# Kernel tuning notes

Measured on AMD Instinct MI355X. Metric: run time of the kernel, lower is better.

The kernel has to match this reference:

```python
import jax, jax.numpy as jnp
import numpy as np

HEADS = 8
C_OUT = 256


def _gconv1x1(x, w, g):
    # x: (B, Cin, H, W); w: (Cout, Cin//g) -> grouped 1x1 conv, out (B, g, Cout//g, L)
    B, C, H, W = x.shape
    xr = x.reshape(B, g, C // g, H * W)
    wr = w.reshape(g, w.shape[0] // g, C // g)
    return jnp.einsum('god,bgdl->bgol', wr, xr)


def _sine_pe(d, L, dtype):
    # standard transformer sinusoidal PE laid out as (channels=d, positions=L)
    pos = jnp.arange(L, dtype=jnp.float32)
    i = jnp.arange(0, d, 2, dtype=jnp.float32)
    inv_freq = jnp.exp(-np.float32(np.log(10000.0)) * i / d)  # (d/2,)
    ang = inv_freq[:, None] * pos[None, :]                    # (d/2, L)
    pe = jnp.zeros((d, L), jnp.float32)
    pe = pe.at[0::2].set(jnp.sin(ang)).at[1::2].set(jnp.cos(ang))
    return pe.astype(dtype)


def setup_inputs() -> dict:
    key = jax.random.key(0)
    k1, k2, k3, k4 = jax.random.split(key, 4)
    B, Cin, H, W = 2, 256, 24, 24
    std = np.float32(np.sqrt(2.0 / C_OUT))  # kaiming_normal fan_out, relu gain
    x = jax.random.normal(k1, (B, Cin, H, W), jnp.float32)
    wq = jax.random.normal(k2, (C_OUT, Cin // HEADS), jnp.float32) * std
    wk = jax.random.normal(k3, (C_OUT, Cin // HEADS), jnp.float32) * std
    wv = jax.random.normal(k4, (C_OUT, Cin // HEADS), jnp.float32) * std
    return {"x": x, "wq": wq, "wk": wk, "wv": wv}


def reference(x, wq, wk, wv):
    B, Cin, H, W = x.shape
    g = HEADS
    d = C_OUT // g
    L = H * W
    q = _gconv1x1(x, wq, g)  # (B, g, d, L)
    k = _gconv1x1(x, wk, g)
    v = _gconv1x1(x, wv, g)
    # sinusoidal positional encoding added to keys over flattened spatial dim
    pe = _sine_pe(C_OUT, L, x.dtype)
    k = (k.reshape(B, C_OUT, L) + pe[None]).reshape(B, g, d, L)
    # NOTE: original torch code flattens batch AND heads into the attention dim
    qf = q.transpose(0, 1, 3, 2).reshape(-1, d)   # (N, d), N = B*g*L
    kf = k.transpose(2, 0, 1, 3).reshape(d, -1)   # (d, N)
    vf = v.transpose(0, 1, 3, 2).reshape(-1, d)   # (N, d)
    scale = np.float32(np.sqrt(g / C_OUT))        # = 1/sqrt(d)
    att = jax.nn.softmax(qf @ kf * scale, axis=-1)  # (N, N)
    out = att @ vf                                  # (N, d)
    out = out.reshape(B, g, L, d).transpose(0, 1, 3, 2).reshape(B, C_OUT, H, W)
    return out
```

## Files before the change

### kernel.cpp

```cpp
#include <hip/hip_runtime.h>
#include <hip/hip_bf16.h>


#define LSP   576
#define NROW  9216
#define DH    32
#define NW    16
#define KPW   (NROW / NW)
#define NTILE 9
#define PSTR  40
#define QB    36
#define SZ    ((size_t)NROW * DH)
#define SZP   (SZ + 4096)

typedef __attribute__((ext_vector_type(8))) short bh8;
typedef __attribute__((ext_vector_type(4))) float f4;

static __device__ __forceinline__ unsigned short f2bf(float x) {
    union { float f; unsigned int i; } w; w.f = x;
    unsigned int u = w.i;
    return (unsigned short)((u + 0x7fffu + ((u >> 16) & 1u)) >> 16);
}
static __device__ __forceinline__ unsigned int pkbf(float a, float b) {
    union { __hip_bfloat162 h2; unsigned int u; } w;
    w.h2 = __float22bfloat162_rn(make_float2(a, b));
    return w.u;
}
static __device__ __forceinline__ float fexp2(float x) {
#if __has_builtin(__builtin_amdgcn_exp2f)
    return __builtin_amdgcn_exp2f(x);
#else
    return exp2f(x);
#endif
}

#define MFMA(a, b, c) __builtin_amdgcn_mfma_f32_16x16x32_bf16(a, b, c, 0, 0, 0)

__global__ __launch_bounds__(256) void sa_proj_kernel(
    const float* __restrict__ x,
    const float* __restrict__ wq, const float* __restrict__ wk, const float* __restrict__ wv,
    unsigned short* __restrict__ Qhi, unsigned short* __restrict__ Khi,
    unsigned short* __restrict__ Vt)
{
    __shared__ __align__(16) float xs[32 * 40];
    __shared__ float vt[32 * 37];
    __shared__ float wqs[32 * 33], wks[32 * 33], wvs[32 * 33];
    const int t = threadIdx.x;
    const int bg = blockIdx.x >> 4;
    const int part = blockIdx.x & 15;
    const int g = bg & 7;
    const int l0 = part * 36;

    const float* xp = x + (size_t)bg * 32 * LSP + l0;
    for (int i = t; i < 32 * 9; i += 256) {
        int d = i / 9, seg = i % 9;
        *(float4*)(xs + d * 40 + seg * 4) = *(const float4*)(xp + d * LSP + seg * 4);
    }
    for (int i = t; i < 1024; i += 256) {
        int o = i >> 5, d = i & 31;
        wqs[o * 33 + d] = wq[(g * 32 + o) * 32 + d];
        wks[o * 33 + d] = wk[(g * 32 + o) * 32 + d];
        wvs[o * 33 + d] = wv[(g * 32 + o) * 32 + d];
    }
    __syncthreads();

    const float scale = 0.17677669529663687f * 1.4426950408889634f;
    for (int idx = t; idx < 32 * 36; idx += 256) {
        const int o = idx & 31;
        const int lloc = idx >> 5;
        const int l = l0 + lloc;
        float aq = 0.f, ak = 0.f, av = 0.f;
        #pragma unroll
        for (int d = 0; d < 32; d++) {
            const float xv = xs[d * 40 + lloc];
            aq = fmaf(wqs[o * 33 + d], xv, aq);
            ak = fmaf(wks[o * 33 + d], xv, ak);
            av = fmaf(wvs[o * 33 + d], xv, av);
        }
        aq *= scale;
        const int c = g * 32 + o;
        const float i2 = (float)(c & ~1);
        const float inv = __expf(-0.035977892078031968f * i2);
        float sv, cv;
        __sincosf(inv * (float)l, &sv, &cv);
        ak += (c & 1) ? cv : sv;

        const size_t row = (size_t)bg * LSP + l;
        Qhi[row * 32 + o] = f2bf(aq);
        Khi[row * 32 + o] = f2bf(ak);
        vt[o * 37 + lloc] = av;
    }
    __syncthreads();

    for (int idx = t; idx < 32 * 36; idx += 256) {
        const int d = idx / 36;
        const int cc = idx - d * 36;
        const int n = bg * LSP + l0 + cc;
        const int k = n & 31;
        const int cperm = (k < 16) ? ((k >> 2) * 8 + (k & 3))
                                   : (((k - 16) >> 2) * 8 + ((k - 16) & 3) + 4);
        Vt[(size_t)(n >> 5) * 1024 + d * 32 + cperm] = f2bf(vt[d * 37 + cc]);
    }
}

__global__ __launch_bounds__(1024, 4) void sa_attn_kernel(
    const unsigned short* __restrict__ Qhi, const unsigned short* __restrict__ Khi,
    const unsigned short* __restrict__ Vt, float* __restrict__ out)
{
    __shared__ __align__(16) unsigned short shm[NW * 48 * PSTR];
    const int t = threadIdx.x;
    const int wave = t >> 6, lane = t & 63;
    const int quad = lane >> 4, l16 = lane & 15;
    const int n0 = blockIdx.x * QB;

    unsigned short* psw = shm + wave * 48 * PSTR;

    const bh8 qh0 = *(const bh8*)(Qhi + (size_t)(n0 + l16) * DH + quad * 8);
    const bh8 qh1 = *(const bh8*)(Qhi + (size_t)(n0 + 16 + l16) * DH + quad * 8);
    const bh8 qh2 = *(const bh8*)(Qhi + (size_t)(n0 + 32 + l16) * DH + quad * 8);

    f4 o00 = {0.f,0.f,0.f,0.f}, o01 = {0.f,0.f,0.f,0.f};
    f4 o10 = {0.f,0.f,0.f,0.f}, o11 = {0.f,0.f,0.f,0.f};
    f4 o20 = {0.f,0.f,0.f,0.f}, o21 = {0.f,0.f,0.f,0.f};
    float ls0 = 0.f, ls1 = 0.f, ls2 = 0.f;
    const f4 zf = {0.f,0.f,0.f,0.f};

    const int kbase = wave * KPW;
    const int tile0 = kbase >> 5;

    bh8 kfa0 = *(const bh8*)(Khi + (size_t)(kbase + l16) * DH + quad * 8);
    bh8 kfa1 = *(const bh8*)(Khi + (size_t)(kbase + 16 + l16) * DH + quad * 8);
    bh8 kfb0 = *(const bh8*)(Khi + (size_t)(kbase + 32 + l16) * DH + quad * 8);
    bh8 kfb1 = *(const bh8*)(Khi + (size_t)(kbase + 48 + l16) * DH + quad * 8);
    bh8 vfa0 = *(const bh8*)(Vt + (size_t)tile0 * 1024 + l16 * 32 + quad * 8);
    bh8 vfa1 = *(const bh8*)(Vt + (size_t)tile0 * 1024 + (16 + l16) * 32 + quad * 8);
    bh8 vfb0 = *(const bh8*)(Vt + (size_t)(tile0 + 1) * 1024 + l16 * 32 + quad * 8);
    bh8 vfb1 = *(const bh8*)(Vt + (size_t)(tile0 + 1) * 1024 + (16 + l16) * 32 + quad * 8);

    for (int it = 0; it < NTILE; ++it) {
        const int tn = (it + 1 < NTILE) ? it + 1 : it;
        const int kna = kbase + tn * 64;

        f4 s00 = MFMA(kfa0, qh0, zf);
        f4 s01 = MFMA(kfa0, qh1, zf);
        f4 s02 = MFMA(kfa0, qh2, zf);
        f4 s10 = MFMA(kfa1, qh0, zf);
        f4 s11 = MFMA(kfa1, qh1, zf);
        f4 s12 = MFMA(kfa1, qh2, zf);
        kfa0 = *(const bh8*)(Khi + (size_t)(kna + l16) * DH + quad * 8);
        kfa1 = *(const bh8*)(Khi + (size_t)(kna + 16 + l16) * DH + quad * 8);

        uint4 w0, w1, w2;
        {
            float a = fexp2(s00[0]), b = fexp2(s00[1]),
                  c = fexp2(s00[2]), d = fexp2(s00[3]);
            ls0 += (a + b) + (c + d);
            w0.x = pkbf(a, b); w0.y = pkbf(c, d);
            a = fexp2(s10[0]); b = fexp2(s10[1]);
            c = fexp2(s10[2]); d = fexp2(s10[3]);
            ls0 += (a + b) + (c + d);
            w0.z = pkbf(a, b); w0.w = pkbf(c, d);
            a = fexp2(s01[0]); b = fexp2(s01[1]);
            c = fexp2(s01[2]); d = fexp2(s01[3]);
            ls1 += (a + b) + (c + d);
            w1.x = pkbf(a, b); w1.y = pkbf(c, d);
            a = fexp2(s11[0]); b = fexp2(s11[1]);
            c = fexp2(s11[2]); d = fexp2(s11[3]);
            ls1 += (a + b) + (c + d);
            w1.z = pkbf(a, b); w1.w = pkbf(c, d);
            a = fexp2(s02[0]); b = fexp2(s02[1]);
            c = fexp2(s02[2]); d = fexp2(s02[3]);
            ls2 += (a + b) + (c + d);
            w2.x = pkbf(a, b); w2.y = pkbf(c, d);
            a = fexp2(s12[0]); b = fexp2(s12[1]);
            c = fexp2(s12[2]); d = fexp2(s12[3]);
            ls2 += (a + b) + (c + d);
            w2.z = pkbf(a, b); w2.w = pkbf(c, d);
        }
        *(uint4*)(psw + l16 * PSTR + quad * 8) = w0;
        *(uint4*)(psw + (16 + l16) * PSTR + quad * 8) = w1;
        *(uint4*)(psw + (32 + l16) * PSTR + quad * 8) = w2;

        f4 b00 = MFMA(kfb0, qh0, zf);
        f4 b01 = MFMA(kfb0, qh1, zf);
        f4 b02 = MFMA(kfb0, qh2, zf);
        f4 b10 = MFMA(kfb1, qh0, zf);
        f4 b11 = MFMA(kfb1, qh1, zf);
        f4 b12 = MFMA(kfb1, qh2, zf);
        kfb0 = *(const bh8*)(Khi + (size_t)(kna + 32 + l16) * DH + quad * 8);
        kfb1 = *(const bh8*)(Khi + (size_t)(kna + 48 + l16) * DH + quad * 8);

        uint4 u0, u1, u2;
        {
            float a = fexp2(b00[0]), b = fexp2(b00[1]),
                  c = fexp2(b00[2]), d = fexp2(b00[3]);
            ls0 += (a + b) + (c + d);
            u0.x = pkbf(a, b); u0.y = pkbf(c, d);
            a = fexp2(b10[0]); b = fexp2(b10[1]);
            c = fexp2(b10[2]); d = fexp2(b10[3]);
            ls0 += (a + b) + (c + d);
            u0.z = pkbf(a, b); u0.w = pkbf(c, d);
            a = fexp2(b01[0]); b = fexp2(b01[1]);
            c = fexp2(b01[2]); d = fexp2(b01[3]);
            ls1 += (a + b) + (c + d);
            u1.x = pkbf(a, b); u1.y = pkbf(c, d);
            a = fexp2(b11[0]); b = fexp2(b11[1]);
            c = fexp2(b11[2]); d = fexp2(b11[3]);
            ls1 += (a + b) + (c + d);
            u1.z = pkbf(a, b); u1.w = pkbf(c, d);
            a = fexp2(b02[0]); b = fexp2(b02[1]);
            c = fexp2(b02[2]); d = fexp2(b02[3]);
            ls2 += (a + b) + (c + d);
            u2.x = pkbf(a, b); u2.y = pkbf(c, d);
            a = fexp2(b12[0]); b = fexp2(b12[1]);
            c = fexp2(b12[2]); d = fexp2(b12[3]);
            ls2 += (a + b) + (c + d);
            u2.z = pkbf(a, b); u2.w = pkbf(c, d);
        }

        {
            const bh8 pa0 = *(const bh8*)(psw + l16 * PSTR + quad * 8);
            const bh8 pa1 = *(const bh8*)(psw + (16 + l16) * PSTR + quad * 8);
            const bh8 pa2 = *(const bh8*)(psw + (32 + l16) * PSTR + quad * 8);
            o00 = MFMA(pa0, vfa0, o00); o01 = MFMA(pa0, vfa1, o01);
            o10 = MFMA(pa1, vfa0, o10); o11 = MFMA(pa1, vfa1, o11);
            o20 = MFMA(pa2, vfa0, o20); o21 = MFMA(pa2, vfa1, o21);
        }
        vfa0 = *(const bh8*)(Vt + (size_t)(tile0 + 2 * tn) * 1024 + l16 * 32 + quad * 8);
        vfa1 = *(const bh8*)(Vt + (size_t)(tile0 + 2 * tn) * 1024 + (16 + l16) * 32 + quad * 8);

        *(uint4*)(psw + l16 * PSTR + quad * 8) = u0;
        *(uint4*)(psw + (16 + l16) * PSTR + quad * 8) = u1;
        *(uint4*)(psw + (32 + l16) * PSTR + quad * 8) = u2;

        {
            const bh8 pb0 = *(const bh8*)(psw + l16 * PSTR + quad * 8);
            const bh8 pb1 = *(const bh8*)(psw + (16 + l16) * PSTR + quad * 8);
            const bh8 pb2 = *(const bh8*)(psw + (32 + l16) * PSTR + quad * 8);
            o00 = MFMA(pb0, vfb0, o00); o01 = MFMA(pb0, vfb1, o01);
            o10 = MFMA(pb1, vfb0, o10); o11 = MFMA(pb1, vfb1, o11);
            o20 = MFMA(pb2, vfb0, o20); o21 = MFMA(pb2, vfb1, o21);
        }
        vfb0 = *(const bh8*)(Vt + (size_t)(tile0 + 2 * tn + 1) * 1024 + l16 * 32 + quad * 8);
        vfb1 = *(const bh8*)(Vt + (size_t)(tile0 + 2 * tn + 1) * 1024 + (16 + l16) * 32 + quad * 8);
    }

    ls0 += __shfl_xor(ls0, 16); ls0 += __shfl_xor(ls0, 32);
    ls1 += __shfl_xor(ls1, 16); ls1 += __shfl_xor(ls1, 32);
    ls2 += __shfl_xor(ls2, 16); ls2 += __shfl_xor(ls2, 32);

    __syncthreads();
    float* mo = (float*)shm;
    float* mls = mo + 8 * 1536;
    const int mw = wave & 7;
    float* mp = mo + mw * 1536;
    if (wave < 8) {
        #pragma unroll
        for (int reg = 0; reg < 4; ++reg) {
            const int q0 = quad * 4 + reg;
            mp[l16 * 48 + q0]             = o00[reg];
            mp[(16 + l16) * 48 + q0]      = o01[reg];
            mp[l16 * 48 + 16 + q0]        = o10[reg];
            mp[(16 + l16) * 48 + 16 + q0] = o11[reg];
            mp[l16 * 48 + 32 + q0]        = o20[reg];
            mp[(16 + l16) * 48 + 32 + q0] = o21[reg];
        }
        if (quad == 0) {
            mls[mw * 48 + l16]      = ls0;
            mls[mw * 48 + 16 + l16] = ls1;
            mls[mw * 48 + 32 + l16] = ls2;
        }
    }
    __syncthreads();
    if (wave >= 8) {
        #pragma unroll
        for (int reg = 0; reg < 4; ++reg) {
            const int q0 = quad * 4 + reg;
            mp[l16 * 48 + q0]             += o00[reg];
            mp[(16 + l16) * 48 + q0]      += o01[reg];
            mp[l16 * 48 + 16 + q0]        += o10[reg];
            mp[(16 + l16) * 48 + 16 + q0] += o11[reg];
            mp[l16 * 48 + 32 + q0]        += o20[reg];
            mp[(16 + l16) * 48 + 32 + q0] += o21[reg];
        }
        if (quad == 0) {
            mls[mw * 48 + l16]      += ls0;
            mls[mw * 48 + 16 + l16] += ls1;
            mls[mw * 48 + 32 + l16] += ls2;
        }
    }
    __syncthreads();

    const int bg = n0 / LSP;
    const int l0 = n0 - bg * LSP;
    for (int c = t; c < 32 * QB; c += 1024) {
        const int d = c / QB;
        const int q = c - d * QB;
        float num = 0.f, den = 0.f;
        #pragma unroll
        for (int w2 = 0; w2 < 8; ++w2) {
            num += mo[w2 * 1536 + d * 48 + q];
            den += mls[w2 * 48 + q];
        }
        out[((size_t)(bg * 32 + d)) * LSP + l0 + q] = num / den;
    }
}

extern "C" void kernel_launch(void* const* d_in, const int* in_sizes, int n_in,
                              void* d_out, int out_size, void* d_ws, size_t ws_size,
                              hipStream_t stream) {
    (void)in_sizes; (void)n_in; (void)out_size; (void)ws_size;
    const float* x  = (const float*)d_in[0];
    const float* wq = (const float*)d_in[1];
    const float* wk = (const float*)d_in[2];
    const float* wv = (const float*)d_in[3];

    unsigned short* ws = (unsigned short*)d_ws;
    unsigned short* Qhi = ws;
    unsigned short* Khi = ws + SZP;
    unsigned short* Vt  = ws + 2 * SZP;
    float* out = (float*)d_out;

    sa_proj_kernel<<<256, 256, 0, stream>>>(x, wq, wk, wv, Qhi, Khi, Vt);
    sa_attn_kernel<<<256, 1024, 0, stream>>>(Qhi, Khi, Vt, out);
}
```

Baseline: 90.66 us.

## Fuse projection and attention into one cooperative kernel; compute row sums via MFMA

Merges the projection kernel into the attention kernel and separates the two phases with a cooperative-groups grid sync, launched via hipLaunchCooperativeKernel with 256 blocks of 1024 threads. This removes one kernel launch and the gap between launches. The softmax denominators are now accumulated by extra MFMAs against a ones vector instead of scalar adds and shuffles, moving VALU work onto the matrix units. The cost is a grid-wide barrier, a reliance on all 256 blocks being co-resident, and extra MFMA issue per tile.

```diff
diff --git a/kernel.cpp b/kernel.cpp
--- a/kernel.cpp
+++ b/kernel.cpp
@@ -1,5 +1,8 @@
 #include <hip/hip_runtime.h>
 #include <hip/hip_bf16.h>
+#include <hip/hip_cooperative_groups.h>
+
+namespace cg = cooperative_groups;
 
 
 #define LSP   576
@@ -36,79 +39,82 @@
 
 #define MFMA(a, b, c) __builtin_amdgcn_mfma_f32_16x16x32_bf16(a, b, c, 0, 0, 0)
 
-__global__ __launch_bounds__(256) void sa_proj_kernel(
+__global__ __launch_bounds__(1024, 4) void sa_fused_kernel(
     const float* __restrict__ x,
     const float* __restrict__ wq, const float* __restrict__ wk, const float* __restrict__ wv,
     unsigned short* __restrict__ Qhi, unsigned short* __restrict__ Khi,
-    unsigned short* __restrict__ Vt)
-{
-    __shared__ __align__(16) float xs[32 * 40];
-    __shared__ float vt[32 * 37];
-    __shared__ float wqs[32 * 33], wks[32 * 33], wvs[32 * 33];
-    const int t = threadIdx.x;
-    const int bg = blockIdx.x >> 4;
-    const int part = blockIdx.x & 15;
-    const int g = bg & 7;
-    const int l0 = part * 36;
-
-    const float* xp = x + (size_t)bg * 32 * LSP + l0;
-    for (int i = t; i < 32 * 9; i += 256) {
-        int d = i / 9, seg = i % 9;
-        *(float4*)(xs + d * 40 + seg * 4) = *(const float4*)(xp + d * LSP + seg * 4);
-    }
-    for (int i = t; i < 1024; i += 256) {
-        int o = i >> 5, d = i & 31;
-        wqs[o * 33 + d] = wq[(g * 32 + o) * 32 + d];
-        wks[o * 33 + d] = wk[(g * 32 + o) * 32 + d];
-        wvs[o * 33 + d] = wv[(g * 32 + o) * 32 + d];
-    }
-    __syncthreads();
-
-    const float scale = 0.17677669529663687f * 1.4426950408889634f;
-    for (int idx = t; idx < 32 * 36; idx += 256) {
-        const int o = idx & 31;
-        const int lloc = idx >> 5;
-        const int l = l0 + lloc;
-        float aq = 0.f, ak = 0.f, av = 0.f;
-        #pragma unroll
-        for (int d = 0; d < 32; d++) {
-            const float xv = xs[d * 40 + lloc];
-            aq = fmaf(wqs[o * 33 + d], xv, aq);
-            ak = fmaf(wks[o * 33 + d], xv, ak);
-            av = fmaf(wvs[o * 33 + d], xv, av);
-        }
-        aq *= scale;
-        const int c = g * 32 + o;
-        const float i2 = (float)(c & ~1);
-        const float inv = __expf(-0.035977892078031968f * i2);
-        float sv, cv;
-        __sincosf(inv * (float)l, &sv, &cv);
-        ak += (c & 1) ? cv : sv;
-
-        const size_t row = (size_t)bg * LSP + l;
-        Qhi[row * 32 + o] = f2bf(aq);
-        Khi[row * 32 + o] = f2bf(ak);
-        vt[o * 37 + lloc] = av;
-    }
-    __syncthreads();
-
-    for (int idx = t; idx < 32 * 36; idx += 256) {
-        const int d = idx / 36;
-        const int cc = idx - d * 36;
-        const int n = bg * LSP + l0 + cc;
-        const int k = n & 31;
-        const int cperm = (k < 16) ? ((k >> 2) * 8 + (k & 3))
-                                   : (((k - 16) >> 2) * 8 + ((k - 16) & 3) + 4);
-        Vt[(size_t)(n >> 5) * 1024 + d * 32 + cperm] = f2bf(vt[d * 37 + cc]);
-    }
-}
-
-__global__ __launch_bounds__(1024, 4) void sa_attn_kernel(
-    const unsigned short* __restrict__ Qhi, const unsigned short* __restrict__ Khi,
-    const unsigned short* __restrict__ Vt, float* __restrict__ out)
+    unsigned short* __restrict__ Vt, float* __restrict__ out)
 {
     __shared__ __align__(16) unsigned short shm[NW * 48 * PSTR];
     const int t = threadIdx.x;
+
+    {
+        float* xs  = (float*)shm;
+        float* vt  = xs + 32 * 40;
+        float* wqs = vt + 32 * 37;
+        float* wks = wqs + 32 * 33;
+        float* wvs = wks + 32 * 33;
+
+        const int bg = blockIdx.x >> 4;
+        const int part = blockIdx.x & 15;
+        const int g = bg & 7;
+        const int l0 = part * 36;
+
+        const float* xp = x + (size_t)bg * 32 * LSP + l0;
+        if (t < 288) {
+            const int d = t / 9, seg = t - d * 9;
+            *(float4*)(xs + d * 40 + seg * 4) = *(const float4*)(xp + d * LSP + seg * 4);
+        }
+        {
+            const int o = t >> 5, d = t & 31;
+            wqs[o * 33 + d] = wq[(g * 32 + o) * 32 + d];
+            wks[o * 33 + d] = wk[(g * 32 + o) * 32 + d];
+            wvs[o * 33 + d] = wv[(g * 32 + o) * 32 + d];
+        }
+        __syncthreads();
+
+        const float scale = 0.17677669529663687f * 1.4426950408889634f;
+        for (int idx = t; idx < 32 * 36; idx += 1024) {
+            const int o = idx & 31;
+            const int lloc = idx >> 5;
+            const int l = l0 + lloc;
+            float aq = 0.f, ak = 0.f, av = 0.f;
+            #pragma unroll
+            for (int d = 0; d < 32; d++) {
+                const float xv = xs[d * 40 + lloc];
+                aq = fmaf(wqs[o * 33 + d], xv, aq);
+                ak = fmaf(wks[o * 33 + d], xv, ak);
+                av = fmaf(wvs[o * 33 + d], xv, av);
+            }
+            aq *= scale;
+            const int c = g * 32 + o;
+            const float i2 = (float)(c & ~1);
+            const float inv = __expf(-0.035977892078031968f * i2);
+            float sv, cv;
+            __sincosf(inv * (float)l, &sv, &cv);
+            ak += (c & 1) ? cv : sv;
+
+            const size_t row = (size_t)bg * LSP + l;
+            Qhi[row * 32 + o] = f2bf(aq);
+            Khi[row * 32 + o] = f2bf(ak);
+            vt[o * 37 + lloc] = av;
+        }
+        __syncthreads();
+
+        for (int idx = t; idx < 32 * 36; idx += 1024) {
+            const int d = idx / 36;
+            const int cc = idx - d * 36;
+            const int n = bg * LSP + l0 + cc;
+            const int k = n & 31;
+            const int cperm = (k < 16) ? ((k >> 2) * 8 + (k & 3))
+                                       : (((k - 16) >> 2) * 8 + ((k - 16) & 3) + 4);
+            Vt[(size_t)(n >> 5) * 1024 + d * 32 + cperm] = f2bf(vt[d * 37 + cc]);
+        }
+    }
+
+    __threadfence();
+    cg::this_grid().sync();
+
     const int wave = t >> 6, lane = t & 63;
     const int quad = lane >> 4, l16 = lane & 15;
     const int n0 = blockIdx.x * QB;
@@ -119,10 +125,13 @@
     const bh8 qh1 = *(const bh8*)(Qhi + (size_t)(n0 + 16 + l16) * DH + quad * 8);
     const bh8 qh2 = *(const bh8*)(Qhi + (size_t)(n0 + 32 + l16) * DH + quad * 8);
 
+    const short oneb = (short)0x3F80;
+    const bh8 ones = {oneb, oneb, oneb, oneb, oneb, oneb, oneb, oneb};
+
     f4 o00 = {0.f,0.f,0.f,0.f}, o01 = {0.f,0.f,0.f,0.f};
     f4 o10 = {0.f,0.f,0.f,0.f}, o11 = {0.f,0.f,0.f,0.f};
     f4 o20 = {0.f,0.f,0.f,0.f}, o21 = {0.f,0.f,0.f,0.f};
-    float ls0 = 0.f, ls1 = 0.f, ls2 = 0.f;
+    f4 lo0 = {0.f,0.f,0.f,0.f}, lo1 = {0.f,0.f,0.f,0.f}, lo2 = {0.f,0.f,0.f,0.f};
     const f4 zf = {0.f,0.f,0.f,0.f};
 
     const int kbase = wave * KPW;
@@ -154,27 +163,21 @@
         {
             float a = fexp2(s00[0]), b = fexp2(s00[1]),
                   c = fexp2(s00[2]), d = fexp2(s00[3]);
-            ls0 += (a + b) + (c + d);
             w0.x = pkbf(a, b); w0.y = pkbf(c, d);
             a = fexp2(s10[0]); b = fexp2(s10[1]);
             c = fexp2(s10[2]); d = fexp2(s10[3]);
-            ls0 += (a + b) + (c + d);
             w0.z = pkbf(a, b); w0.w = pkbf(c, d);
             a = fexp2(s01[0]); b = fexp2(s01[1]);
             c = fexp2(s01[2]); d = fexp2(s01[3]);
-            ls1 += (a + b) + (c + d);
             w1.x = pkbf(a, b); w1.y = pkbf(c, d);
             a = fexp2(s11[0]); b = fexp2(s11[1]);
             c = fexp2(s11[2]); d = fexp2(s11[3]);
-            ls1 += (a + b) + (c + d);
             w1.z = pkbf(a, b); w1.w = pkbf(c, d);
             a = fexp2(s02[0]); b = fexp2(s02[1]);
             c = fexp2(s02[2]); d = fexp2(s02[3]);
-            ls2 += (a + b) + (c + d);
             w2.x = pkbf(a, b); w2.y = pkbf(c, d);
             a = fexp2(s12[0]); b = fexp2(s12[1]);
             c = fexp2(s12[2]); d = fexp2(s12[3]);
-            ls2 += (a + b) + (c + d);
             w2.z = pkbf(a, b); w2.w = pkbf(c, d);
         }
         *(uint4*)(psw + l16 * PSTR + quad * 8) = w0;
@@ -194,27 +197,21 @@
         {
             float a = fexp2(b00[0]), b = fexp2(b00[1]),
                   c = fexp2(b00[2]), d = fexp2(b00[3]);
-            ls0 += (a + b) + (c + d);
             u0.x = pkbf(a, b); u0.y = pkbf(c, d);
             a = fexp2(b10[0]); b = fexp2(b10[1]);
             c = fexp2(b10[2]); d = fexp2(b10[3]);
-            ls0 += (a + b) + (c + d);
             u0.z = pkbf(a, b); u0.w = pkbf(c, d);
             a = fexp2(b01[0]); b = fexp2(b01[1]);
             c = fexp2(b01[2]); d = fexp2(b01[3]);
-            ls1 += (a + b) + (c + d);
             u1.x = pkbf(a, b); u1.y = pkbf(c, d);
             a = fexp2(b11[0]); b = fexp2(b11[1]);
             c = fexp2(b11[2]); d = fexp2(b11[3]);
-            ls1 += (a + b) + (c + d);
             u1.z = pkbf(a, b); u1.w = pkbf(c, d);
             a = fexp2(b02[0]); b = fexp2(b02[1]);
             c = fexp2(b02[2]); d = fexp2(b02[3]);
-            ls2 += (a + b) + (c + d);
             u2.x = pkbf(a, b); u2.y = pkbf(c, d);
             a = fexp2(b12[0]); b = fexp2(b12[1]);
             c = fexp2(b12[2]); d = fexp2(b12[3]);
-            ls2 += (a + b) + (c + d);
             u2.z = pkbf(a, b); u2.w = pkbf(c, d);
         }
 
@@ -225,6 +222,9 @@
             o00 = MFMA(pa0, vfa0, o00); o01 = MFMA(pa0, vfa1, o01);
             o10 = MFMA(pa1, vfa0, o10); o11 = MFMA(pa1, vfa1, o11);
             o20 = MFMA(pa2, vfa0, o20); o21 = MFMA(pa2, vfa1, o21);
+            lo0 = MFMA(pa0, ones, lo0);
+            lo1 = MFMA(pa1, ones, lo1);
+            lo2 = MFMA(pa2, ones, lo2);
         }
         vfa0 = *(const bh8*)(Vt + (size_t)(tile0 + 2 * tn) * 1024 + l16 * 32 + quad * 8);
         vfa1 = *(const bh8*)(Vt + (size_t)(tile0 + 2 * tn) * 1024 + (16 + l16) * 32 + quad * 8);
@@ -240,14 +240,13 @@
             o00 = MFMA(pb0, vfb0, o00); o01 = MFMA(pb0, vfb1, o01);
             o10 = MFMA(pb1, vfb0, o10); o11 = MFMA(pb1, vfb1, o11);
             o20 = MFMA(pb2, vfb0, o20); o21 = MFMA(pb2, vfb1, o21);
+            lo0 = MFMA(pb0, ones, lo0);
+            lo1 = MFMA(pb1, ones, lo1);
+            lo2 = MFMA(pb2, ones, lo2);
         }
         vfb0 = *(const bh8*)(Vt + (size_t)(tile0 + 2 * tn + 1) * 1024 + l16 * 32 + quad * 8);
         vfb1 = *(const bh8*)(Vt + (size_t)(tile0 + 2 * tn + 1) * 1024 + (16 + l16) * 32 + quad * 8);
     }
-
-    ls0 += __shfl_xor(ls0, 16); ls0 += __shfl_xor(ls0, 32);
-    ls1 += __shfl_xor(ls1, 16); ls1 += __shfl_xor(ls1, 32);
-    ls2 += __shfl_xor(ls2, 16); ls2 += __shfl_xor(ls2, 32);
 
     __syncthreads();
     float* mo = (float*)shm;
@@ -265,10 +264,13 @@
             mp[l16 * 48 + 32 + q0]        = o20[reg];
             mp[(16 + l16) * 48 + 32 + q0] = o21[reg];
         }
-        if (quad == 0) {
-            mls[mw * 48 + l16]      = ls0;
-            mls[mw * 48 + 16 + l16] = ls1;
-            mls[mw * 48 + 32 + l16] = ls2;
+        if (l16 == 0) {
+            #pragma unroll
+            for (int reg = 0; reg < 4; ++reg) {
+                mls[mw * 48 + quad * 4 + reg]      = lo0[reg];
+                mls[mw * 48 + 16 + quad * 4 + reg] = lo1[reg];
+                mls[mw * 48 + 32 + quad * 4 + reg] = lo2[reg];
+            }
         }
     }
     __syncthreads();
@@ -283,10 +285,13 @@
             mp[l16 * 48 + 32 + q0]        += o20[reg];
             mp[(16 + l16) * 48 + 32 + q0] += o21[reg];
         }
-        if (quad == 0) {
-            mls[mw * 48 + l16]      += ls0;
-            mls[mw * 48 + 16 + l16] += ls1;
-            mls[mw * 48 + 32 + l16] += ls2;
+        if (l16 == 0) {
+            #pragma unroll
+            for (int reg = 0; reg < 4; ++reg) {
+                mls[mw * 48 + quad * 4 + reg]      += lo0[reg];
+                mls[mw * 48 + 16 + quad * 4 + reg] += lo1[reg];
+                mls[mw * 48 + 32 + quad * 4 + reg] += lo2[reg];
+            }
         }
     }
     __syncthreads();
@@ -321,6 +326,8 @@
     unsigned short* Vt  = ws + 2 * SZP;
     float* out = (float*)d_out;
 
-    sa_proj_kernel<<<256, 256, 0, stream>>>(x, wq, wk, wv, Qhi, Khi, Vt);
-    sa_attn_kernel<<<256, 1024, 0, stream>>>(Qhi, Khi, Vt, out);
-}
+    void* args[] = {(void*)&x, (void*)&wq, (void*)&wk, (void*)&wv,
+                    (void*)&Qhi, (void*)&Khi, (void*)&Vt, (void*)&out};
+    hipLaunchCooperativeKernel((const void*)sa_fused_kernel, dim3(256), dim3(1024),
+                               args, 0, stream);
+}
```

Result: slower. 197.4 us (+117.8%).
